# Kernel tuning notes

Measured on AMD Instinct MI355X. Metric: run time of the kernel, lower is better.

Reference implementation:

```python
import jax, jax.numpy as jnp
import numpy as np


def setup_inputs() -> dict:
    key = jax.random.key(0)
    k1, k2, k3, k4 = jax.random.split(key, 4)
    B, S, C = 16, 2048, 512
    x = jax.random.normal(k1, (B, S, C), dtype=jnp.float32)
    x_prime = jax.random.normal(k2, (B, S, C), dtype=jnp.float32)
    W = jax.random.normal(k3, (C, C), dtype=jnp.float32) * (1.0 / np.sqrt(C))
    b = jax.random.normal(k4, (C,), dtype=jnp.float32) * 0.01
    return {"x": x, "x_prime": x_prime, "W": W, "b": b}


def reference(x, x_prime, W, b):
    # q = Linear(x_prime): [B, S, C]
    q = jnp.einsum("bsc,dc->bsd", x_prime, W) + b
    # score = tanh(x_prime) @ q^T : [B, S, S]
    score = jnp.einsum("bsc,btc->bst", jnp.tanh(x_prime), q)
    alpha = jax.nn.softmax(score, axis=-1)
    # y_att = alpha @ x : [B, S, C]
    y_att = jnp.einsum("bst,btc->bsc", alpha, x)
    # dropout is identity in eval mode
    return jnp.tanh(y_att)
```

## Files before the change

kernel.cpp:

```cpp
#include <hip/hip_runtime.h>
#include <hip/hip_bf16.h>
#include <math.h>

typedef __bf16 bf16x8 __attribute__((ext_vector_type(8)));
typedef float  f32x4  __attribute__((ext_vector_type(4)));
typedef float  f32x16 __attribute__((ext_vector_type(16)));

#define MFMA16(a, b, c) __builtin_amdgcn_mfma_f32_16x16x32_bf16((a), (b), (c), 0, 0, 0)
#define MFMA32(a, b, c) __builtin_amdgcn_mfma_f32_32x32x16_bf16((a), (b), (c), 0, 0, 0)

static constexpr int    kB  = 16;
static constexpr int    kS  = 2048;
static constexpr int    kC  = 512;
static constexpr size_t kNE = (size_t)kB * kS * kC;

static __device__ __forceinline__ void split_bf16(float v, __bf16 &hi, __bf16 &lo) {
  hi = (__bf16)v;
  lo = (__bf16)(v - (float)hi);
}

static __device__ __forceinline__ int swzb(int row, int e) {
  return ((row << 7) + (e << 1)) ^ ((row & 7) << 4);
}
static __device__ __forceinline__ int swzp(int row, int e) {
  return ((row << 8) + (e << 1)) ^ ((row & 7) << 4);
}

static __device__ __forceinline__ void split_store16_swz(
    float4 v0, float4 v1, float4 v2, float4 v3, char* hi, char* lo, int row, int e0) {
  float vv[16] = {v0.x, v0.y, v0.z, v0.w, v1.x, v1.y, v1.z, v1.w,
                  v2.x, v2.y, v2.z, v2.w, v3.x, v3.y, v3.z, v3.w};
  bf16x8 h0, h1, l0, l1;
#pragma unroll
  for (int i = 0; i < 8; ++i) {
    __bf16 a, b;
    split_bf16(vv[i], a, b);     h0[i] = a; l0[i] = b;
    split_bf16(vv[8 + i], a, b); h1[i] = a; l1[i] = b;
  }
  *(bf16x8*)(hi + swzb(row, e0))     = h0;
  *(bf16x8*)(hi + swzb(row, e0 + 8)) = h1;
  *(bf16x8*)(lo + swzb(row, e0))     = l0;
  *(bf16x8*)(lo + swzb(row, e0 + 8)) = l1;
}

__global__ __launch_bounds__(256) void k_tanh_split(
    const float* __restrict__ xp, __bf16* __restrict__ th, __bf16* __restrict__ tl) {
  size_t i = ((size_t)blockIdx.x * 256 + threadIdx.x) * 8;
  float4 a = *(const float4*)(xp + i);
  float4 b = *(const float4*)(xp + i + 4);
  float v[8] = {a.x, a.y, a.z, a.w, b.x, b.y, b.z, b.w};
  bf16x8 h, l;
#pragma unroll
  for (int k = 0; k < 8; ++k) {
    float t = tanhf(v[k]);
    __bf16 hh, ll;
    split_bf16(t, hh, ll);
    h[k] = hh; l[k] = ll;
  }
  *(bf16x8*)(th + i) = h;
  *(bf16x8*)(tl + i) = l;
}

__global__ __launch_bounds__(256) void k_transpose_x(
    const float* __restrict__ x, __bf16* __restrict__ xbt) {
  __shared__ float tile[64][65];
  int bid = blockIdx.x;
  int b   = bid >> 8;
  int t0  = ((bid >> 3) & 31) * 64;
  int c0  = (bid & 7) * 64;
  int row = threadIdx.x >> 2;
  int seg = threadIdx.x & 3;
  const float* src = x + (size_t)(b * kS + t0 + row) * kC + c0 + seg * 16;
  float4 v0 = *(const float4*)(src + 0);
  float4 v1 = *(const float4*)(src + 4);
  float4 v2 = *(const float4*)(src + 8);
  float4 v3 = *(const float4*)(src + 12);
  float vv[16] = {v0.x, v0.y, v0.z, v0.w, v1.x, v1.y, v1.z, v1.w,
                  v2.x, v2.y, v2.z, v2.w, v3.x, v3.y, v3.z, v3.w};
#pragma unroll
  for (int i = 0; i < 16; ++i) tile[row][seg * 16 + i] = vv[i];
  __syncthreads();
  bf16x8 o0, o1;
#pragma unroll
  for (int i = 0; i < 8; ++i) o0[i] = (__bf16)tile[seg * 16 + i][row];
#pragma unroll
  for (int i = 0; i < 8; ++i) o1[i] = (__bf16)tile[seg * 16 + 8 + i][row];
  __bf16* dst = xbt + (size_t)(b * kC + c0 + row) * kS + t0 + seg * 16;
  *(bf16x8*)(dst)     = o0;
  *(bf16x8*)(dst + 8) = o1;
}

__global__ __launch_bounds__(256) void k_qgemm(
    const float* __restrict__ xp, const float* __restrict__ W,
    const float* __restrict__ bias, __bf16* __restrict__ qh, __bf16* __restrict__ ql) {
  __shared__ __align__(16) char lds[32768];
  char* Ah = lds;
  char* Al = lds + 8192;
  char* Bh = lds + 16384;
  char* Bl = lds + 24576;

  int bid = blockIdx.x;
  int n0  = (bid & 7) * 64;
  int m0  = (bid >> 3) * 64;

  int tid  = threadIdx.x;
  int lane = tid & 63;
  int wave = tid >> 6;
  int qd   = lane >> 4;
  int cl   = lane & 15;
  int row  = tid >> 2;
  int seg  = tid & 3;

  f32x4 acc[4] = {};
  const float* srcA = xp + (size_t)(m0 + row) * kC + seg * 16;
  const float* srcB = W  + (size_t)(n0 + row) * kC + seg * 16;

  float4 va0, va1, va2, va3, vb0, vb1, vb2, vb3;
  auto load_ab = [&](int kc) {
    const float* a = srcA + kc * 64;
    va0 = *(const float4*)(a);      va1 = *(const float4*)(a + 4);
    va2 = *(const float4*)(a + 8);  va3 = *(const float4*)(a + 12);
    const float* bb = srcB + kc * 64;
    vb0 = *(const float4*)(bb);     vb1 = *(const float4*)(bb + 4);
    vb2 = *(const float4*)(bb + 8); vb3 = *(const float4*)(bb + 12);
  };

  load_ab(0);
  for (int kc = 0; kc < 8; ++kc) {
    split_store16_swz(va0, va1, va2, va3, Ah, Al, row, seg * 16);
    split_store16_swz(vb0, vb1, vb2, vb3, Bh, Bl, row, seg * 16);
    __syncthreads();
    if (kc < 7) load_ab(kc + 1);
    __builtin_amdgcn_s_setprio(1);
#pragma unroll
    for (int ks = 0; ks < 2; ++ks) {
      int ka = ks * 32 + qd * 8;
      bf16x8 ah = *(const bf16x8*)(Ah + swzb(wave * 16 + cl, ka));
      bf16x8 al = *(const bf16x8*)(Al + swzb(wave * 16 + cl, ka));
#pragma unroll
      for (int j = 0; j < 4; ++j) {
        bf16x8 bh = *(const bf16x8*)(Bh + swzb(j * 16 + cl, ka));
        bf16x8 bl = *(const bf16x8*)(Bl + swzb(j * 16 + cl, ka));
        acc[j] = MFMA16(ah, bh, acc[j]);
        acc[j] = MFMA16(ah, bl, acc[j]);
        acc[j] = MFMA16(al, bh, acc[j]);
      }
    }
    __builtin_amdgcn_s_setprio(0);
    __syncthreads();
  }
#pragma unroll
  for (int j = 0; j < 4; ++j) {
    int d = n0 + j * 16 + cl;
    float bv = bias[d];
#pragma unroll
    for (int r = 0; r < 4; ++r) {
      int m = m0 + wave * 16 + qd * 4 + r;
      float v = acc[j][r] + bv;
      __bf16 h, l;
      split_bf16(v, h, l);
      qh[(size_t)m * kC + d] = h;
      ql[(size_t)m * kC + d] = l;
    }
  }
}

__global__ __launch_bounds__(256, 2) void k_attn(
    const __bf16* __restrict__ th, const __bf16* __restrict__ tl,
    const __bf16* __restrict__ qh, const __bf16* __restrict__ ql,
    const __bf16* __restrict__ xbt, float* __restrict__ out) {
  __shared__ __align__(16) char lds[49664];
  char* Ah  = lds;
  char* Al  = lds + 8192;
  char* Bh  = lds + 16384;
  char* Bl  = lds + 32768;
  char* P   = lds;
  char* Xt0 = lds + 16384;
  char* Xt1 = lds + 32768;
  float* stat = (float*)(lds + 49152);

  int bid = blockIdx.x;
  int b   = (bid & 7) | ((bid >> 8) << 3);
  int s0  = ((bid >> 3) & 31) * 64;

  int tid  = threadIdx.x;
  int lane = tid & 63;
  int wave = tid >> 6;
  int qd   = lane >> 4;
  int cl   = lane & 15;
  int l31  = lane & 31;
  int lh   = lane >> 5;
  int whalf = wave & 1;
  int wcol  = wave >> 1;

  const float LOG2E = 1.4426950408889634f;

  float m_r[4], l_r[4];
  f32x16 O[8] = {};
#pragma unroll
  for (int r = 0; r < 4; ++r) { m_r[r] = -INFINITY; l_r[r] = 0.f; }

  const size_t rowbase = (size_t)b * kS;

  const int arow = tid >> 2, aseg = tid & 3;
  const int brow = tid >> 1, bseg = tid & 1;
  const int xrow = tid >> 2, xseg = tid & 3;
  const int prow = whalf * 32 + l31;

  for (int tt = 0; tt < 16; ++tt) {
    int t0 = tt * 128;
    f32x4 Sacc[8] = {};
    for (int kc = 0; kc < 8; ++kc) {
      {
        size_t g = (rowbase + s0 + arow) * kC + kc * 64 + aseg * 16;
        bf16x8 h0 = *(const bf16x8*)(th + g), h1 = *(const bf16x8*)(th + g + 8);
        bf16x8 l0 = *(const bf16x8*)(tl + g), l1 = *(const bf16x8*)(tl + g + 8);
        *(bf16x8*)(Ah + swzb(arow, aseg * 16))     = h0;
        *(bf16x8*)(Ah + swzb(arow, aseg * 16 + 8)) = h1;
        *(bf16x8*)(Al + swzb(arow, aseg * 16))     = l0;
        *(bf16x8*)(Al + swzb(arow, aseg * 16 + 8)) = l1;
      }
      {
        size_t g = (rowbase + t0 + brow) * kC + kc * 64 + bseg * 32;
#pragma unroll
        for (int u = 0; u < 4; ++u) {
          bf16x8 vh = *(const bf16x8*)(qh + g + u * 8);
          bf16x8 vl = *(const bf16x8*)(ql + g + u * 8);
          *(bf16x8*)(Bh + swzb(brow, bseg * 32 + u * 8)) = vh;
          *(bf16x8*)(Bl + swzb(brow, bseg * 32 + u * 8)) = vl;
        }
      }
      __syncthreads();
      __builtin_amdgcn_s_setprio(1);
#pragma unroll
      for (int ks = 0; ks < 2; ++ks) {
        int ka = ks * 32 + qd * 8;
        bf16x8 ah = *(const bf16x8*)(Ah + swzb(wave * 16 + cl, ka));
        bf16x8 al = *(const bf16x8*)(Al + swzb(wave * 16 + cl, ka));
#pragma unroll
        for (int j = 0; j < 8; ++j) {
          bf16x8 bh = *(const bf16x8*)(Bh + swzb(j * 16 + cl, ka));
          bf16x8 bl = *(const bf16x8*)(Bl + swzb(j * 16 + cl, ka));
          Sacc[j] = MFMA16(ah, bh, Sacc[j]);
          Sacc[j] = MFMA16(ah, bl, Sacc[j]);
          Sacc[j] = MFMA16(al, bh, Sacc[j]);
        }
      }
      __builtin_amdgcn_s_setprio(0);
      __syncthreads();
    }
    float rmax[4];
#pragma unroll
    for (int r = 0; r < 4; ++r) {
      float v = Sacc[0][r];
#pragma unroll
      for (int j = 1; j < 8; ++j) v = fmaxf(v, Sacc[j][r]);
      rmax[r] = v;
    }
#pragma unroll
    for (int mk = 1; mk < 16; mk <<= 1)
#pragma unroll
      for (int r = 0; r < 4; ++r)
        rmax[r] = fmaxf(rmax[r], __shfl_xor(rmax[r], mk, 64));
    float alpha[4], rsum[4];
#pragma unroll
    for (int r = 0; r < 4; ++r) {
      float mn = fmaxf(m_r[r], rmax[r]);
      alpha[r] = exp2f((m_r[r] - mn) * LOG2E);
      m_r[r] = mn;
      rsum[r] = 0.f;
    }
#pragma unroll
    for (int j = 0; j < 8; ++j)
#pragma unroll
      for (int r = 0; r < 4; ++r) {
        float p = exp2f((Sacc[j][r] - m_r[r]) * LOG2E);
        Sacc[j][r] = p;
        rsum[r] += p;
      }
#pragma unroll
    for (int mk = 1; mk < 16; mk <<= 1)
#pragma unroll
      for (int r = 0; r < 4; ++r)
        rsum[r] += __shfl_xor(rsum[r], mk, 64);
#pragma unroll
    for (int r = 0; r < 4; ++r)
      l_r[r] = l_r[r] * alpha[r] + rsum[r];
    if (cl == 0) {
#pragma unroll
      for (int r = 0; r < 4; ++r) stat[wave * 16 + qd * 4 + r] = alpha[r];
    }
#pragma unroll
    for (int j = 0; j < 8; ++j)
#pragma unroll
      for (int r = 0; r < 4; ++r) {
        int pr = wave * 16 + qd * 4 + r;
        *(__bf16*)(P + swzp(pr, j * 16 + cl)) = (__bf16)Sacc[j][r];
      }
    __syncthreads();
    float ar[16];
#pragma unroll
    for (int i = 0; i < 16; ++i)
      ar[i] = stat[whalf * 32 + (i & 3) + 8 * (i >> 2) + 4 * lh];
    bf16x8 pa[8];
#pragma unroll
    for (int ks = 0; ks < 8; ++ks)
      pa[ks] = *(const bf16x8*)(P + swzp(prow, ks * 16 + lh * 8));
#pragma unroll
    for (int t = 0; t < 8; ++t)
#pragma unroll
      for (int i = 0; i < 16; ++i)
        O[t][i] *= ar[i];
#pragma unroll
    for (int step = 0; step < 4; ++step) {
      {
        size_t g0 = ((size_t)b * kC + step * 64 + xrow) * kS + t0 + xseg * 32;
        size_t g1 = g0 + (size_t)256 * kS;
#pragma unroll
        for (int u = 0; u < 4; ++u)
          *(bf16x8*)(Xt0 + swzp(xrow, xseg * 32 + u * 8)) = *(const bf16x8*)(xbt + g0 + u * 8);
#pragma unroll
        for (int u = 0; u < 4; ++u)
          *(bf16x8*)(Xt1 + swzp(xrow, xseg * 32 + u * 8)) = *(const bf16x8*)(xbt + g1 + u * 8);
      }
      __syncthreads();
      const char* Xt = wcol ? Xt1 : Xt0;
      __builtin_amdgcn_s_setprio(1);
#pragma unroll
      for (int ks = 0; ks < 8; ++ks) {
#pragma unroll
        for (int nloc = 0; nloc < 2; ++nloc) {
          bf16x8 xb = *(const bf16x8*)(Xt + swzp(nloc * 32 + l31, ks * 16 + lh * 8));
          O[step * 2 + nloc] = MFMA32(pa[ks], xb, O[step * 2 + nloc]);
        }
      }
      __builtin_amdgcn_s_setprio(0);
      __syncthreads();
    }
  }
  if (cl == 0) {
#pragma unroll
    for (int r = 0; r < 4; ++r) stat[wave * 16 + qd * 4 + r] = l_r[r];
  }
  __syncthreads();
  float linv[16];
#pragma unroll
  for (int i = 0; i < 16; ++i)
    linv[i] = __builtin_amdgcn_rcpf(stat[whalf * 32 + (i & 3) + 8 * (i >> 2) + 4 * lh]);
#pragma unroll
  for (int t = 0; t < 8; ++t) {
    int colbase = wcol * 256 + (t >> 1) * 64 + (t & 1) * 32 + l31;
#pragma unroll
    for (int i = 0; i < 16; ++i) {
      int rowl = (i & 3) + 8 * (i >> 2) + 4 * lh;
      float v = O[t][i] * linv[i];
      float e = exp2f(2.f * LOG2E * v);
      out[(rowbase + s0 + whalf * 32 + rowl) * kC + colbase] =
          1.f - 2.f * __builtin_amdgcn_rcpf(e + 1.f);
    }
  }
}

extern "C" void kernel_launch(void* const* d_in, const int* in_sizes, int n_in,
                              void* d_out, int out_size, void* d_ws, size_t ws_size,
                              hipStream_t stream) {
  const float* x    = (const float*)d_in[0];
  const float* xp   = (const float*)d_in[1];
  const float* W    = (const float*)d_in[2];
  const float* bias = (const float*)d_in[3];
  float* out = (float*)d_out;

  __bf16* ws  = (__bf16*)d_ws;
  __bf16* th  = ws;
  __bf16* tl  = ws + kNE;
  __bf16* qh  = ws + 2 * kNE;
  __bf16* ql  = ws + 3 * kNE;
  __bf16* xbt = ws + 4 * kNE;

  k_tanh_split<<<8192, 256, 0, stream>>>(xp, th, tl);
  k_transpose_x<<<4096, 256, 0, stream>>>(x, xbt);
  k_qgemm<<<4096, 256, 0, stream>>>(xp, W, bias, qh, ql);
  k_attn<<<512, 256, 0, stream>>>(th, tl, qh, ql, xbt, out);
}
```

Baseline: 1.090 ms.

## Restructure attention kernel with async global-to-LDS double buffering and larger tiles

Rewrites the fused attention kernel to use 512-thread blocks covering 128 query rows, with direct global-to-LDS loads (global_load_lds) that are double-buffered so the next K-chunk and X tiles are fetched while the current MFMAs run. The score GEMM moves from 16x16 to 32x32 MFMA tiles, and row max/sum are combined across wave pairs through LDS. The goal is to hide memory latency and cut register-staged copies and synchronization stalls. In exchange it uses about 160KB of LDS, which limits occupancy, and it launches only 256 blocks, which risks underfilling the GPU.

```diff
diff --git a/kernel.cpp b/kernel.cpp
--- a/kernel.cpp
+++ b/kernel.cpp
@@ -19,11 +19,14 @@
   lo = (__bf16)(v - (float)hi);
 }
 
+static __device__ __forceinline__ void gload16(const void* g, void* l) {
+  __builtin_amdgcn_global_load_lds(
+      (const __attribute__((address_space(1))) char*)g,
+      (__attribute__((address_space(3))) char*)l, 16, 0, 0);
+}
+
 static __device__ __forceinline__ int swzb(int row, int e) {
   return ((row << 7) + (e << 1)) ^ ((row & 7) << 4);
-}
-static __device__ __forceinline__ int swzp(int row, int e) {
-  return ((row << 8) + (e << 1)) ^ ((row & 7) << 4);
 }
 
 static __device__ __forceinline__ void split_store16_swz(
@@ -165,197 +168,203 @@
   }
 }
 
-__global__ __launch_bounds__(256, 2) void k_attn(
+__global__ __launch_bounds__(512, 2) void k_attn(
     const __bf16* __restrict__ th, const __bf16* __restrict__ tl,
     const __bf16* __restrict__ qh, const __bf16* __restrict__ ql,
     const __bf16* __restrict__ xbt, float* __restrict__ out) {
-  __shared__ __align__(16) char lds[49664];
-  char* Ah  = lds;
-  char* Al  = lds + 8192;
-  char* Bh  = lds + 16384;
-  char* Bl  = lds + 32768;
-  char* P   = lds;
-  char* Xt0 = lds + 16384;
-  char* Xt1 = lds + 32768;
-  float* stat = (float*)(lds + 49152);
+  __shared__ __align__(16) char lds[163840];
+  char*  P     = lds + 65536;
+  float* statm = (float*)(lds);
+  float* stats = (float*)(lds + 1024);
+  const int XEVEN = 98304, XODD = 131072;
 
   int bid = blockIdx.x;
-  int b   = (bid & 7) | ((bid >> 8) << 3);
-  int s0  = ((bid >> 3) & 31) * 64;
+  int b   = bid >> 4;
+  int s0  = (bid & 15) * 128;
 
   int tid  = threadIdx.x;
   int lane = tid & 63;
-  int wave = tid >> 6;
-  int qd   = lane >> 4;
-  int cl   = lane & 15;
+  int wv   = tid >> 6;
   int l31  = lane & 31;
   int lh   = lane >> 5;
-  int whalf = wave & 1;
-  int wcol  = wave >> 1;
+  int wg   = wv >> 1;
+  int cg   = wv & 1;
 
   const float LOG2E = 1.4426950408889634f;
 
-  float m_r[4], l_r[4];
+  float m_r[16], l_r[16];
+#pragma unroll
+  for (int i = 0; i < 16; ++i) { m_r[i] = -INFINITY; l_r[i] = 0.f; }
   f32x16 O[8] = {};
-#pragma unroll
-  for (int r = 0; r < 4; ++r) { m_r[r] = -INFINITY; l_r[r] = 0.f; }
-
-  const size_t rowbase = (size_t)b * kS;
-
-  const int arow = tid >> 2, aseg = tid & 3;
-  const int brow = tid >> 1, bseg = tid & 1;
-  const int xrow = tid >> 2, xseg = tid & 3;
-  const int prow = whalf * 32 + l31;
+
+  auto stage_score = [&](int kc, int bufsel, int t0q) {
+    char* Ahd = lds + bufsel * 65536;
+    char* Ald = Ahd + 16384;
+    char* Bhd = Ahd + 32768;
+    char* Bld = Ahd + 49152;
+#pragma unroll
+    for (int u = 0; u < 2; ++u) {
+      int slot = wv * 128 + u * 64 + lane;
+      int r = slot >> 3;
+      int c = (slot & 7) ^ (r & 7);
+      size_t gA = (size_t)(b * kS + s0 + r) * kC + kc * 64 + c * 8;
+      size_t gB = (size_t)(b * kS + t0q + r) * kC + kc * 64 + c * 8;
+      int ldoff = (wv * 128 + u * 64) * 16;
+      gload16(th + gA, Ahd + ldoff);
+      gload16(tl + gA, Ald + ldoff);
+      gload16(qh + gB, Bhd + ldoff);
+      gload16(ql + gB, Bld + ldoff);
+    }
+  };
+  auto stage_xpair = [&](int step, int pairbase, int t0q) {
+#pragma unroll
+    for (int half = 0; half < 2; ++half) {
+      char* dst = lds + pairbase + half * 16384;
+#pragma unroll
+      for (int u = 0; u < 2; ++u) {
+        int slot = wv * 128 + u * 64 + lane;
+        int r = slot >> 4;
+        int c = (slot & 15) ^ (r & 7);
+        size_t g = ((size_t)b * kC + half * 256 + step * 64 + r) * kS + t0q + c * 8;
+        gload16(xbt + g, dst + (wv * 128 + u * 64) * 16);
+      }
+    }
+  };
+
+  stage_score(0, 0, 0);
+  __syncthreads();
+
+  const int arow = wg * 32 + l31;
+  const int prow = wg * 32 + l31;
 
   for (int tt = 0; tt < 16; ++tt) {
     int t0 = tt * 128;
-    f32x4 Sacc[8] = {};
+    f32x16 S0 = {}, S1 = {};
     for (int kc = 0; kc < 8; ++kc) {
-      {
-        size_t g = (rowbase + s0 + arow) * kC + kc * 64 + aseg * 16;
-        bf16x8 h0 = *(const bf16x8*)(th + g), h1 = *(const bf16x8*)(th + g + 8);
-        bf16x8 l0 = *(const bf16x8*)(tl + g), l1 = *(const bf16x8*)(tl + g + 8);
-        *(bf16x8*)(Ah + swzb(arow, aseg * 16))     = h0;
-        *(bf16x8*)(Ah + swzb(arow, aseg * 16 + 8)) = h1;
-        *(bf16x8*)(Al + swzb(arow, aseg * 16))     = l0;
-        *(bf16x8*)(Al + swzb(arow, aseg * 16 + 8)) = l1;
-      }
-      {
-        size_t g = (rowbase + t0 + brow) * kC + kc * 64 + bseg * 32;
-#pragma unroll
-        for (int u = 0; u < 4; ++u) {
-          bf16x8 vh = *(const bf16x8*)(qh + g + u * 8);
-          bf16x8 vl = *(const bf16x8*)(ql + g + u * 8);
-          *(bf16x8*)(Bh + swzb(brow, bseg * 32 + u * 8)) = vh;
-          *(bf16x8*)(Bl + swzb(brow, bseg * 32 + u * 8)) = vl;
-        }
-      }
-      __syncthreads();
+      if (kc < 7) stage_score(kc + 1, (kc + 1) & 1, t0);
+      const char* cb  = lds + (kc & 1) * 65536;
+      const char* cAh = cb, *cAl = cb + 16384, *cBh = cb + 32768, *cBl = cb + 49152;
       __builtin_amdgcn_s_setprio(1);
 #pragma unroll
-      for (int ks = 0; ks < 2; ++ks) {
-        int ka = ks * 32 + qd * 8;
-        bf16x8 ah = *(const bf16x8*)(Ah + swzb(wave * 16 + cl, ka));
-        bf16x8 al = *(const bf16x8*)(Al + swzb(wave * 16 + cl, ka));
-#pragma unroll
-        for (int j = 0; j < 8; ++j) {
-          bf16x8 bh = *(const bf16x8*)(Bh + swzb(j * 16 + cl, ka));
-          bf16x8 bl = *(const bf16x8*)(Bl + swzb(j * 16 + cl, ka));
-          Sacc[j] = MFMA16(ah, bh, Sacc[j]);
-          Sacc[j] = MFMA16(ah, bl, Sacc[j]);
-          Sacc[j] = MFMA16(al, bh, Sacc[j]);
+      for (int ks = 0; ks < 4; ++ks) {
+        int ach = ((ks * 2 + lh) ^ (arow & 7)) * 16;
+        bf16x8 ah = *(const bf16x8*)(cAh + arow * 128 + ach);
+        bf16x8 al = *(const bf16x8*)(cAl + arow * 128 + ach);
+#pragma unroll
+        for (int tile = 0; tile < 2; ++tile) {
+          int trow = cg * 64 + tile * 32 + l31;
+          int bch  = ((ks * 2 + lh) ^ (trow & 7)) * 16;
+          bf16x8 bh = *(const bf16x8*)(cBh + trow * 128 + bch);
+          bf16x8 bl = *(const bf16x8*)(cBl + trow * 128 + bch);
+          if (tile == 0) {
+            S0 = MFMA32(ah, bh, S0); S0 = MFMA32(ah, bl, S0); S0 = MFMA32(al, bh, S0);
+          } else {
+            S1 = MFMA32(ah, bh, S1); S1 = MFMA32(ah, bl, S1); S1 = MFMA32(al, bh, S1);
+          }
         }
       }
       __builtin_amdgcn_s_setprio(0);
       __syncthreads();
     }
-    float rmax[4];
-#pragma unroll
-    for (int r = 0; r < 4; ++r) {
-      float v = Sacc[0][r];
-#pragma unroll
-      for (int j = 1; j < 8; ++j) v = fmaxf(v, Sacc[j][r]);
-      rmax[r] = v;
-    }
-#pragma unroll
-    for (int mk = 1; mk < 16; mk <<= 1)
-#pragma unroll
-      for (int r = 0; r < 4; ++r)
-        rmax[r] = fmaxf(rmax[r], __shfl_xor(rmax[r], mk, 64));
-    float alpha[4], rsum[4];
-#pragma unroll
-    for (int r = 0; r < 4; ++r) {
-      float mn = fmaxf(m_r[r], rmax[r]);
-      alpha[r] = exp2f((m_r[r] - mn) * LOG2E);
-      m_r[r] = mn;
-      rsum[r] = 0.f;
+    float rm[16];
+#pragma unroll
+    for (int i = 0; i < 16; ++i) rm[i] = fmaxf(S0[i], S1[i]);
+#pragma unroll
+    for (int mk = 1; mk < 32; mk <<= 1)
+#pragma unroll
+      for (int i = 0; i < 16; ++i) rm[i] = fmaxf(rm[i], __shfl_xor(rm[i], mk, 64));
+    if (l31 == 0) {
+#pragma unroll
+      for (int i = 0; i < 16; ++i) {
+        int rl = (i & 3) + 8 * (i >> 2) + 4 * lh;
+        statm[cg * 128 + wg * 32 + rl] = rm[i];
+      }
+    }
+    __syncthreads();
+    stage_xpair(0, XEVEN, t0);
+    float alpha[16];
+#pragma unroll
+    for (int i = 0; i < 16; ++i) {
+      int rl = (i & 3) + 8 * (i >> 2) + 4 * lh;
+      float om = statm[(cg ^ 1) * 128 + wg * 32 + rl];
+      float M  = fmaxf(m_r[i], fmaxf(rm[i], om));
+      alpha[i] = exp2f((m_r[i] - M) * LOG2E);
+      m_r[i] = M;
+      l_r[i] *= alpha[i];
     }
 #pragma unroll
     for (int j = 0; j < 8; ++j)
 #pragma unroll
-      for (int r = 0; r < 4; ++r) {
-        float p = exp2f((Sacc[j][r] - m_r[r]) * LOG2E);
-        Sacc[j][r] = p;
-        rsum[r] += p;
-      }
-#pragma unroll
-    for (int mk = 1; mk < 16; mk <<= 1)
-#pragma unroll
-      for (int r = 0; r < 4; ++r)
-        rsum[r] += __shfl_xor(rsum[r], mk, 64);
-#pragma unroll
-    for (int r = 0; r < 4; ++r)
-      l_r[r] = l_r[r] * alpha[r] + rsum[r];
-    if (cl == 0) {
-#pragma unroll
-      for (int r = 0; r < 4; ++r) stat[wave * 16 + qd * 4 + r] = alpha[r];
-    }
-#pragma unroll
-    for (int j = 0; j < 8; ++j)
-#pragma unroll
-      for (int r = 0; r < 4; ++r) {
-        int pr = wave * 16 + qd * 4 + r;
-        *(__bf16*)(P + swzp(pr, j * 16 + cl)) = (__bf16)Sacc[j][r];
-      }
-    __syncthreads();
-    float ar[16];
-#pragma unroll
-    for (int i = 0; i < 16; ++i)
-      ar[i] = stat[whalf * 32 + (i & 3) + 8 * (i >> 2) + 4 * lh];
+      for (int i = 0; i < 16; ++i) O[j][i] *= alpha[i];
+    float rs[16];
+#pragma unroll
+    for (int i = 0; i < 16; ++i) {
+      S0[i] = exp2f((S0[i] - m_r[i]) * LOG2E);
+      S1[i] = exp2f((S1[i] - m_r[i]) * LOG2E);
+      rs[i] = S0[i] + S1[i];
+    }
+#pragma unroll
+    for (int mk = 1; mk < 32; mk <<= 1)
+#pragma unroll
+      for (int i = 0; i < 16; ++i) rs[i] += __shfl_xor(rs[i], mk, 64);
+    if (l31 == 0) {
+#pragma unroll
+      for (int i = 0; i < 16; ++i) {
+        int rl = (i & 3) + 8 * (i >> 2) + 4 * lh;
+        stats[cg * 128 + wg * 32 + rl] = rs[i];
+      }
+    }
+#pragma unroll
+    for (int tile = 0; tile < 2; ++tile)
+#pragma unroll
+      for (int i = 0; i < 16; ++i) {
+        int s = wg * 32 + (i & 3) + 8 * (i >> 2) + 4 * lh;
+        int t = cg * 64 + tile * 32 + l31;
+        int off = s * 256 + ((((t >> 3) ^ (s & 7)) << 4) | ((t & 7) << 1));
+        *(__bf16*)(P + off) = (__bf16)(tile ? S1[i] : S0[i]);
+      }
+    __syncthreads();
+#pragma unroll
+    for (int i = 0; i < 16; ++i) {
+      int rl = (i & 3) + 8 * (i >> 2) + 4 * lh;
+      l_r[i] += rs[i] + stats[(cg ^ 1) * 128 + wg * 32 + rl];
+    }
     bf16x8 pa[8];
 #pragma unroll
-    for (int ks = 0; ks < 8; ++ks)
-      pa[ks] = *(const bf16x8*)(P + swzp(prow, ks * 16 + lh * 8));
-#pragma unroll
-    for (int t = 0; t < 8; ++t)
-#pragma unroll
-      for (int i = 0; i < 16; ++i)
-        O[t][i] *= ar[i];
+    for (int ks = 0; ks < 8; ++ks) {
+      int ch = ((ks * 2 + lh) ^ (prow & 7)) * 16;
+      pa[ks] = *(const bf16x8*)(P + prow * 256 + ch);
+    }
+    __syncthreads();
 #pragma unroll
     for (int step = 0; step < 4; ++step) {
-      {
-        size_t g0 = ((size_t)b * kC + step * 64 + xrow) * kS + t0 + xseg * 32;
-        size_t g1 = g0 + (size_t)256 * kS;
-#pragma unroll
-        for (int u = 0; u < 4; ++u)
-          *(bf16x8*)(Xt0 + swzp(xrow, xseg * 32 + u * 8)) = *(const bf16x8*)(xbt + g0 + u * 8);
-#pragma unroll
-        for (int u = 0; u < 4; ++u)
-          *(bf16x8*)(Xt1 + swzp(xrow, xseg * 32 + u * 8)) = *(const bf16x8*)(xbt + g1 + u * 8);
-      }
-      __syncthreads();
-      const char* Xt = wcol ? Xt1 : Xt0;
+      if (step < 3)      stage_xpair(step + 1, ((step + 1) & 1) ? XODD : XEVEN, t0);
+      else if (tt < 15)  stage_score(0, 0, t0 + 128);
+      const char* xbb = lds + ((step & 1) ? XODD : XEVEN) + cg * 16384;
       __builtin_amdgcn_s_setprio(1);
 #pragma unroll
-      for (int ks = 0; ks < 8; ++ks) {
-#pragma unroll
-        for (int nloc = 0; nloc < 2; ++nloc) {
-          bf16x8 xb = *(const bf16x8*)(Xt + swzp(nloc * 32 + l31, ks * 16 + lh * 8));
-          O[step * 2 + nloc] = MFMA32(pa[ks], xb, O[step * 2 + nloc]);
+      for (int ks = 0; ks < 8; ++ks)
+#pragma unroll
+        for (int tile = 0; tile < 2; ++tile) {
+          int xrow = tile * 32 + l31;
+          int ch = ((ks * 2 + lh) ^ (xrow & 7)) * 16;
+          bf16x8 xb = *(const bf16x8*)(xbb + xrow * 256 + ch);
+          O[step * 2 + tile] = MFMA32(pa[ks], xb, O[step * 2 + tile]);
         }
-      }
       __builtin_amdgcn_s_setprio(0);
       __syncthreads();
     }
   }
-  if (cl == 0) {
-#pragma unroll
-    for (int r = 0; r < 4; ++r) stat[wave * 16 + qd * 4 + r] = l_r[r];
-  }
-  __syncthreads();
-  float linv[16];
-#pragma unroll
-  for (int i = 0; i < 16; ++i)
-    linv[i] = __builtin_amdgcn_rcpf(stat[whalf * 32 + (i & 3) + 8 * (i >> 2) + 4 * lh]);
-#pragma unroll
-  for (int t = 0; t < 8; ++t) {
-    int colbase = wcol * 256 + (t >> 1) * 64 + (t & 1) * 32 + l31;
-#pragma unroll
-    for (int i = 0; i < 16; ++i) {
-      int rowl = (i & 3) + 8 * (i >> 2) + 4 * lh;
-      float v = O[t][i] * linv[i];
+#pragma unroll
+  for (int i = 0; i < 16; ++i) {
+    int rl = (i & 3) + 8 * (i >> 2) + 4 * lh;
+    float inv = __builtin_amdgcn_rcpf(l_r[i]);
+    size_t rowoff = ((size_t)b * kS + s0 + wg * 32 + rl) * kC;
+#pragma unroll
+    for (int j = 0; j < 8; ++j) {
+      float v = O[j][i] * inv;
       float e = exp2f(2.f * LOG2E * v);
-      out[(rowbase + s0 + whalf * 32 + rowl) * kC + colbase] =
+      out[rowoff + cg * 256 + (j >> 1) * 64 + (j & 1) * 32 + l31] =
           1.f - 2.f * __builtin_amdgcn_rcpf(e + 1.f);
     }
   }
@@ -380,5 +389,5 @@
   k_tanh_split<<<8192, 256, 0, stream>>>(xp, th, tl);
   k_transpose_x<<<4096, 256, 0, stream>>>(x, xbt);
   k_qgemm<<<4096, 256, 0, stream>>>(xp, W, bias, qh, ql);
-  k_attn<<<512, 256, 0, stream>>>(th, tl, qh, ql, xbt, out);
-}
+  k_attn<<<256, 512, 0, stream>>>(th, tl, qh, ql, xbt, out);
+}
```

Result: slower. 1.124 ms (+3.1%).

## Switch attention to fp16 MFMA with two-term Q split and retiled waves

Applied to the files above, without the earlier changes.

Moves all intermediate operands from bf16 to fp16. tanh(x') is now stored as a single fp16 value, and Q keeps a hi/lo split, so the score GEMM needs two MFMAs per tile instead of three, and the tanh low-part buffer is dropped. The attention kernel is retiled so each wave computes a 64x32 score slice and a 64x128 output slice with 16x16x32 f16 MFMAs. Row max and row sum are now combined across waves through LDS, which adds an extra barrier. Accuracy now depends on fp16 range and the reduced split precision.

```diff
diff --git a/kernel.cpp b/kernel.cpp
--- a/kernel.cpp
+++ b/kernel.cpp
@@ -2,12 +2,12 @@
 #include <hip/hip_bf16.h>
 #include <math.h>
 
-typedef __bf16 bf16x8 __attribute__((ext_vector_type(8)));
-typedef float  f32x4  __attribute__((ext_vector_type(4)));
-typedef float  f32x16 __attribute__((ext_vector_type(16)));
+typedef __bf16    bf16x8 __attribute__((ext_vector_type(8)));
+typedef _Float16  f16x8  __attribute__((ext_vector_type(8)));
+typedef float     f32x4  __attribute__((ext_vector_type(4)));
 
 #define MFMA16(a, b, c) __builtin_amdgcn_mfma_f32_16x16x32_bf16((a), (b), (c), 0, 0, 0)
-#define MFMA32(a, b, c) __builtin_amdgcn_mfma_f32_32x32x16_bf16((a), (b), (c), 0, 0, 0)
+#define MFMAH(a, b, c)  __builtin_amdgcn_mfma_f32_16x16x32_f16((a), (b), (c), 0, 0, 0)
 
 static constexpr int    kB  = 16;
 static constexpr int    kS  = 2048;
@@ -21,9 +21,6 @@
 
 static __device__ __forceinline__ int swzb(int row, int e) {
   return ((row << 7) + (e << 1)) ^ ((row & 7) << 4);
-}
-static __device__ __forceinline__ int swzp(int row, int e) {
-  return ((row << 8) + (e << 1)) ^ ((row & 7) << 4);
 }
 
 static __device__ __forceinline__ void split_store16_swz(
@@ -43,26 +40,20 @@
   *(bf16x8*)(lo + swzb(row, e0 + 8)) = l1;
 }
 
-__global__ __launch_bounds__(256) void k_tanh_split(
-    const float* __restrict__ xp, __bf16* __restrict__ th, __bf16* __restrict__ tl) {
+__global__ __launch_bounds__(256) void k_tanh_f16(
+    const float* __restrict__ xp, _Float16* __restrict__ th) {
   size_t i = ((size_t)blockIdx.x * 256 + threadIdx.x) * 8;
   float4 a = *(const float4*)(xp + i);
   float4 b = *(const float4*)(xp + i + 4);
   float v[8] = {a.x, a.y, a.z, a.w, b.x, b.y, b.z, b.w};
-  bf16x8 h, l;
-#pragma unroll
-  for (int k = 0; k < 8; ++k) {
-    float t = tanhf(v[k]);
-    __bf16 hh, ll;
-    split_bf16(t, hh, ll);
-    h[k] = hh; l[k] = ll;
-  }
-  *(bf16x8*)(th + i) = h;
-  *(bf16x8*)(tl + i) = l;
+  f16x8 h;
+#pragma unroll
+  for (int k = 0; k < 8; ++k) h[k] = (_Float16)tanhf(v[k]);
+  *(f16x8*)(th + i) = h;
 }
 
 __global__ __launch_bounds__(256) void k_transpose_x(
-    const float* __restrict__ x, __bf16* __restrict__ xbt) {
+    const float* __restrict__ x, _Float16* __restrict__ xbt) {
   __shared__ float tile[64][65];
   int bid = blockIdx.x;
   int b   = bid >> 8;
@@ -80,19 +71,19 @@
 #pragma unroll
   for (int i = 0; i < 16; ++i) tile[row][seg * 16 + i] = vv[i];
   __syncthreads();
-  bf16x8 o0, o1;
-#pragma unroll
-  for (int i = 0; i < 8; ++i) o0[i] = (__bf16)tile[seg * 16 + i][row];
-#pragma unroll
-  for (int i = 0; i < 8; ++i) o1[i] = (__bf16)tile[seg * 16 + 8 + i][row];
-  __bf16* dst = xbt + (size_t)(b * kC + c0 + row) * kS + t0 + seg * 16;
-  *(bf16x8*)(dst)     = o0;
-  *(bf16x8*)(dst + 8) = o1;
+  f16x8 o0, o1;
+#pragma unroll
+  for (int i = 0; i < 8; ++i) o0[i] = (_Float16)tile[seg * 16 + i][row];
+#pragma unroll
+  for (int i = 0; i < 8; ++i) o1[i] = (_Float16)tile[seg * 16 + 8 + i][row];
+  _Float16* dst = xbt + (size_t)(b * kC + c0 + row) * kS + t0 + seg * 16;
+  *(f16x8*)(dst)     = o0;
+  *(f16x8*)(dst + 8) = o1;
 }
 
 __global__ __launch_bounds__(256) void k_qgemm(
     const float* __restrict__ xp, const float* __restrict__ W,
-    const float* __restrict__ bias, __bf16* __restrict__ qh, __bf16* __restrict__ ql) {
+    const float* __restrict__ bias, _Float16* __restrict__ qh, _Float16* __restrict__ ql) {
   __shared__ __align__(16) char lds[32768];
   char* Ah = lds;
   char* Al = lds + 8192;
@@ -157,8 +148,8 @@
     for (int r = 0; r < 4; ++r) {
       int m = m0 + wave * 16 + qd * 4 + r;
       float v = acc[j][r] + bv;
-      __bf16 h, l;
-      split_bf16(v, h, l);
+      _Float16 h = (_Float16)v;
+      _Float16 l = (_Float16)(v - (float)h);
       qh[(size_t)m * kC + d] = h;
       ql[(size_t)m * kC + d] = l;
     }
@@ -166,199 +157,219 @@
 }
 
 __global__ __launch_bounds__(256, 2) void k_attn(
-    const __bf16* __restrict__ th, const __bf16* __restrict__ tl,
-    const __bf16* __restrict__ qh, const __bf16* __restrict__ ql,
-    const __bf16* __restrict__ xbt, float* __restrict__ out) {
-  __shared__ __align__(16) char lds[49664];
-  char* Ah  = lds;
-  char* Al  = lds + 8192;
-  char* Bh  = lds + 16384;
-  char* Bl  = lds + 32768;
-  char* P   = lds;
-  char* Xt0 = lds + 16384;
-  char* Xt1 = lds + 32768;
-  float* stat = (float*)(lds + 49152);
+    const _Float16* __restrict__ th, const _Float16* __restrict__ qh,
+    const _Float16* __restrict__ ql, const _Float16* __restrict__ xbt,
+    float* __restrict__ out) {
+  __shared__ __align__(16) char lds[59392];
+  char*  Ta    = lds;
+  char*  Qh    = lds + 8192;
+  char*  Ql    = lds + 24576;
+  char*  Xt    = lds;
+  char*  P     = lds + 40960;
+  float* statm = (float*)(lds + 57344);
+  float* stats = (float*)(lds + 58368);
 
   int bid = blockIdx.x;
-  int b   = (bid & 7) | ((bid >> 8) << 3);
-  int s0  = ((bid >> 3) & 31) * 64;
+  int swz = (bid & 7) * 64 + (bid >> 3);
+  int b   = swz >> 5;
+  int s0  = (swz & 31) * 64;
 
   int tid  = threadIdx.x;
   int lane = tid & 63;
-  int wave = tid >> 6;
+  int wv   = tid >> 6;
   int qd   = lane >> 4;
   int cl   = lane & 15;
-  int l31  = lane & 31;
-  int lh   = lane >> 5;
-  int whalf = wave & 1;
-  int wcol  = wave >> 1;
 
   const float LOG2E = 1.4426950408889634f;
 
-  float m_r[4], l_r[4];
-  f32x16 O[8] = {};
-#pragma unroll
-  for (int r = 0; r < 4; ++r) { m_r[r] = -INFINITY; l_r[r] = 0.f; }
-
-  const size_t rowbase = (size_t)b * kS;
-
-  const int arow = tid >> 2, aseg = tid & 3;
-  const int brow = tid >> 1, bseg = tid & 1;
-  const int xrow = tid >> 2, xseg = tid & 3;
-  const int prow = whalf * 32 + l31;
+  float m_r[16], l_r[16];
+#pragma unroll
+  for (int i = 0; i < 16; ++i) { m_r[i] = -INFINITY; l_r[i] = 0.f; }
+  f32x4 O[4][8] = {};
+
+  auto stage_score = [&](int kc, int t0) {
+    {
+      int ar = tid >> 2, as = tid & 3;
+      const _Float16* ga = th + (size_t)(b * kS + s0 + ar) * kC + kc * 64 + as * 16;
+      f16x8 a0 = *(const f16x8*)ga;
+      f16x8 a1 = *(const f16x8*)(ga + 8);
+      *(f16x8*)(Ta + ar * 128 + (((as * 2)     ^ (ar & 7)) << 4)) = a0;
+      *(f16x8*)(Ta + ar * 128 + (((as * 2 + 1) ^ (ar & 7)) << 4)) = a1;
+    }
+    {
+      int qr = tid >> 1, qs = tid & 1;
+      size_t gq = (size_t)(b * kS + t0 + qr) * kC + kc * 64 + qs * 32;
+#pragma unroll
+      for (int u = 0; u < 4; ++u) {
+        f16x8 vh = *(const f16x8*)(qh + gq + u * 8);
+        f16x8 vl = *(const f16x8*)(ql + gq + u * 8);
+        int cc = (((qs * 4 + u) ^ (qr & 7)) << 4);
+        *(f16x8*)(Qh + qr * 128 + cc) = vh;
+        *(f16x8*)(Ql + qr * 128 + cc) = vl;
+      }
+    }
+  };
+  auto stage_x = [&](int sub, int t0) {
+#pragma unroll
+    for (int u = 0; u < 2; ++u) {
+      int r = tid * 2 + u;
+      const _Float16* gx = xbt + (size_t)(b * kC + r) * kS + t0 + sub * 32;
+#pragma unroll
+      for (int j = 0; j < 4; ++j) {
+        f16x8 v = *(const f16x8*)(gx + j * 8);
+        int cc = ((j ^ (r & 3) ^ ((r >> 2) & 3)) << 4);
+        *(f16x8*)(Xt + r * 64 + cc) = v;
+      }
+    }
+  };
 
   for (int tt = 0; tt < 16; ++tt) {
     int t0 = tt * 128;
-    f32x4 Sacc[8] = {};
+    f32x4 S[4][2] = {};
     for (int kc = 0; kc < 8; ++kc) {
-      {
-        size_t g = (rowbase + s0 + arow) * kC + kc * 64 + aseg * 16;
-        bf16x8 h0 = *(const bf16x8*)(th + g), h1 = *(const bf16x8*)(th + g + 8);
-        bf16x8 l0 = *(const bf16x8*)(tl + g), l1 = *(const bf16x8*)(tl + g + 8);
-        *(bf16x8*)(Ah + swzb(arow, aseg * 16))     = h0;
-        *(bf16x8*)(Ah + swzb(arow, aseg * 16 + 8)) = h1;
-        *(bf16x8*)(Al + swzb(arow, aseg * 16))     = l0;
-        *(bf16x8*)(Al + swzb(arow, aseg * 16 + 8)) = l1;
-      }
-      {
-        size_t g = (rowbase + t0 + brow) * kC + kc * 64 + bseg * 32;
-#pragma unroll
-        for (int u = 0; u < 4; ++u) {
-          bf16x8 vh = *(const bf16x8*)(qh + g + u * 8);
-          bf16x8 vl = *(const bf16x8*)(ql + g + u * 8);
-          *(bf16x8*)(Bh + swzb(brow, bseg * 32 + u * 8)) = vh;
-          *(bf16x8*)(Bl + swzb(brow, bseg * 32 + u * 8)) = vl;
-        }
-      }
+      stage_score(kc, t0);
       __syncthreads();
       __builtin_amdgcn_s_setprio(1);
 #pragma unroll
       for (int ks = 0; ks < 2; ++ks) {
-        int ka = ks * 32 + qd * 8;
-        bf16x8 ah = *(const bf16x8*)(Ah + swzb(wave * 16 + cl, ka));
-        bf16x8 al = *(const bf16x8*)(Al + swzb(wave * 16 + cl, ka));
-#pragma unroll
-        for (int j = 0; j < 8; ++j) {
-          bf16x8 bh = *(const bf16x8*)(Bh + swzb(j * 16 + cl, ka));
-          bf16x8 bl = *(const bf16x8*)(Bl + swzb(j * 16 + cl, ka));
-          Sacc[j] = MFMA16(ah, bh, Sacc[j]);
-          Sacc[j] = MFMA16(ah, bl, Sacc[j]);
-          Sacc[j] = MFMA16(al, bh, Sacc[j]);
+        f16x8 ta[4], qbh[2], qbl[2];
+#pragma unroll
+        for (int mt = 0; mt < 4; ++mt) {
+          int rr = mt * 16 + cl;
+          ta[mt] = *(const f16x8*)(Ta + rr * 128 + ((((ks * 4 + qd) ^ (rr & 7))) << 4));
         }
+#pragma unroll
+        for (int nt = 0; nt < 2; ++nt) {
+          int rr = wv * 32 + nt * 16 + cl;
+          int cc = ((((ks * 4 + qd) ^ (rr & 7))) << 4);
+          qbh[nt] = *(const f16x8*)(Qh + rr * 128 + cc);
+          qbl[nt] = *(const f16x8*)(Ql + rr * 128 + cc);
+        }
+#pragma unroll
+        for (int mt = 0; mt < 4; ++mt)
+#pragma unroll
+          for (int nt = 0; nt < 2; ++nt) {
+            S[mt][nt] = MFMAH(ta[mt], qbh[nt], S[mt][nt]);
+            S[mt][nt] = MFMAH(ta[mt], qbl[nt], S[mt][nt]);
+          }
       }
       __builtin_amdgcn_s_setprio(0);
       __syncthreads();
     }
-    float rmax[4];
-#pragma unroll
-    for (int r = 0; r < 4; ++r) {
-      float v = Sacc[0][r];
-#pragma unroll
-      for (int j = 1; j < 8; ++j) v = fmaxf(v, Sacc[j][r]);
-      rmax[r] = v;
-    }
+    float rm[16];
+#pragma unroll
+    for (int mt = 0; mt < 4; ++mt)
+#pragma unroll
+      for (int r = 0; r < 4; ++r)
+        rm[mt * 4 + r] = fmaxf(S[mt][0][r], S[mt][1][r]);
 #pragma unroll
     for (int mk = 1; mk < 16; mk <<= 1)
 #pragma unroll
-      for (int r = 0; r < 4; ++r)
-        rmax[r] = fmaxf(rmax[r], __shfl_xor(rmax[r], mk, 64));
-    float alpha[4], rsum[4];
-#pragma unroll
-    for (int r = 0; r < 4; ++r) {
-      float mn = fmaxf(m_r[r], rmax[r]);
-      alpha[r] = exp2f((m_r[r] - mn) * LOG2E);
-      m_r[r] = mn;
-      rsum[r] = 0.f;
-    }
-#pragma unroll
-    for (int j = 0; j < 8; ++j)
+      for (int i = 0; i < 16; ++i) rm[i] = fmaxf(rm[i], __shfl_xor(rm[i], mk, 64));
+    if (cl == 0) {
+#pragma unroll
+      for (int mt = 0; mt < 4; ++mt)
+#pragma unroll
+        for (int r = 0; r < 4; ++r)
+          statm[(mt * 16 + qd * 4 + r) * 4 + wv] = rm[mt * 4 + r];
+    }
+    __syncthreads();
+    float alpha[16];
+#pragma unroll
+    for (int mt = 0; mt < 4; ++mt)
 #pragma unroll
       for (int r = 0; r < 4; ++r) {
-        float p = exp2f((Sacc[j][r] - m_r[r]) * LOG2E);
-        Sacc[j][r] = p;
-        rsum[r] += p;
+        int i = mt * 4 + r;
+        f32x4 pm = *(const f32x4*)&statm[(mt * 16 + qd * 4 + r) * 4];
+        float M = fmaxf(fmaxf(fmaxf(pm[0], pm[1]), fmaxf(pm[2], pm[3])), m_r[i]);
+        alpha[i] = exp2f((m_r[i] - M) * LOG2E);
+        m_r[i] = M;
+      }
+    float rs[16];
+#pragma unroll
+    for (int mt = 0; mt < 4; ++mt)
+#pragma unroll
+      for (int r = 0; r < 4; ++r) {
+        int i = mt * 4 + r;
+        float p0 = exp2f((S[mt][0][r] - m_r[i]) * LOG2E);
+        float p1 = exp2f((S[mt][1][r] - m_r[i]) * LOG2E);
+        S[mt][0][r] = p0; S[mt][1][r] = p1;
+        rs[i] = p0 + p1;
       }
 #pragma unroll
     for (int mk = 1; mk < 16; mk <<= 1)
 #pragma unroll
-      for (int r = 0; r < 4; ++r)
-        rsum[r] += __shfl_xor(rsum[r], mk, 64);
-#pragma unroll
-    for (int r = 0; r < 4; ++r)
-      l_r[r] = l_r[r] * alpha[r] + rsum[r];
+      for (int i = 0; i < 16; ++i) rs[i] += __shfl_xor(rs[i], mk, 64);
     if (cl == 0) {
 #pragma unroll
-      for (int r = 0; r < 4; ++r) stat[wave * 16 + qd * 4 + r] = alpha[r];
-    }
-#pragma unroll
-    for (int j = 0; j < 8; ++j)
+      for (int mt = 0; mt < 4; ++mt)
+#pragma unroll
+        for (int r = 0; r < 4; ++r)
+          stats[(mt * 16 + qd * 4 + r) * 4 + wv] = rs[mt * 4 + r];
+    }
+#pragma unroll
+    for (int mt = 0; mt < 4; ++mt)
+#pragma unroll
+      for (int nt = 0; nt < 2; ++nt)
+#pragma unroll
+        for (int r = 0; r < 4; ++r) {
+          int row = mt * 16 + qd * 4 + r;
+          int col = wv * 32 + nt * 16 + cl;
+          int off = row * 256 + ((((col >> 3) ^ (row & 7)) << 4)) + ((col & 7) << 1);
+          *(_Float16*)(P + off) = (_Float16)S[mt][nt][r];
+        }
+#pragma unroll
+    for (int mt = 0; mt < 4; ++mt)
+#pragma unroll
+      for (int nt = 0; nt < 8; ++nt)
+#pragma unroll
+        for (int r = 0; r < 4; ++r)
+          O[mt][nt][r] *= alpha[mt * 4 + r];
+    __syncthreads();
+#pragma unroll
+    for (int mt = 0; mt < 4; ++mt)
 #pragma unroll
       for (int r = 0; r < 4; ++r) {
-        int pr = wave * 16 + qd * 4 + r;
-        *(__bf16*)(P + swzp(pr, j * 16 + cl)) = (__bf16)Sacc[j][r];
-      }
-    __syncthreads();
-    float ar[16];
-#pragma unroll
-    for (int i = 0; i < 16; ++i)
-      ar[i] = stat[whalf * 32 + (i & 3) + 8 * (i >> 2) + 4 * lh];
-    bf16x8 pa[8];
-#pragma unroll
-    for (int ks = 0; ks < 8; ++ks)
-      pa[ks] = *(const bf16x8*)(P + swzp(prow, ks * 16 + lh * 8));
-#pragma unroll
-    for (int t = 0; t < 8; ++t)
-#pragma unroll
-      for (int i = 0; i < 16; ++i)
-        O[t][i] *= ar[i];
-#pragma unroll
-    for (int step = 0; step < 4; ++step) {
-      {
-        size_t g0 = ((size_t)b * kC + step * 64 + xrow) * kS + t0 + xseg * 32;
-        size_t g1 = g0 + (size_t)256 * kS;
-#pragma unroll
-        for (int u = 0; u < 4; ++u)
-          *(bf16x8*)(Xt0 + swzp(xrow, xseg * 32 + u * 8)) = *(const bf16x8*)(xbt + g0 + u * 8);
-#pragma unroll
-        for (int u = 0; u < 4; ++u)
-          *(bf16x8*)(Xt1 + swzp(xrow, xseg * 32 + u * 8)) = *(const bf16x8*)(xbt + g1 + u * 8);
-      }
+        int i = mt * 4 + r;
+        f32x4 ps = *(const f32x4*)&stats[(mt * 16 + qd * 4 + r) * 4];
+        l_r[i] = l_r[i] * alpha[i] + (ps[0] + ps[1] + ps[2] + ps[3]);
+      }
+#pragma unroll
+    for (int sub = 0; sub < 4; ++sub) {
+      stage_x(sub, t0);
       __syncthreads();
-      const char* Xt = wcol ? Xt1 : Xt0;
+      f16x8 pa[4];
+#pragma unroll
+      for (int mt = 0; mt < 4; ++mt) {
+        int row = mt * 16 + cl;
+        pa[mt] = *(const f16x8*)(P + row * 256 + ((((sub * 4 + qd) ^ (row & 7))) << 4));
+      }
       __builtin_amdgcn_s_setprio(1);
 #pragma unroll
-      for (int ks = 0; ks < 8; ++ks) {
-#pragma unroll
-        for (int nloc = 0; nloc < 2; ++nloc) {
-          bf16x8 xb = *(const bf16x8*)(Xt + swzp(nloc * 32 + l31, ks * 16 + lh * 8));
-          O[step * 2 + nloc] = MFMA32(pa[ks], xb, O[step * 2 + nloc]);
-        }
+      for (int nt = 0; nt < 8; ++nt) {
+        int xr = wv * 128 + nt * 16 + cl;
+        f16x8 xb = *(const f16x8*)(Xt + xr * 64 + ((qd ^ (xr & 3) ^ ((xr >> 2) & 3)) << 4));
+#pragma unroll
+        for (int mt = 0; mt < 4; ++mt)
+          O[mt][nt] = MFMAH(pa[mt], xb, O[mt][nt]);
       }
       __builtin_amdgcn_s_setprio(0);
       __syncthreads();
     }
   }
-  if (cl == 0) {
-#pragma unroll
-    for (int r = 0; r < 4; ++r) stat[wave * 16 + qd * 4 + r] = l_r[r];
-  }
-  __syncthreads();
-  float linv[16];
-#pragma unroll
-  for (int i = 0; i < 16; ++i)
-    linv[i] = __builtin_amdgcn_rcpf(stat[whalf * 32 + (i & 3) + 8 * (i >> 2) + 4 * lh]);
-#pragma unroll
-  for (int t = 0; t < 8; ++t) {
-    int colbase = wcol * 256 + (t >> 1) * 64 + (t & 1) * 32 + l31;
-#pragma unroll
-    for (int i = 0; i < 16; ++i) {
-      int rowl = (i & 3) + 8 * (i >> 2) + 4 * lh;
-      float v = O[t][i] * linv[i];
-      float e = exp2f(2.f * LOG2E * v);
-      out[(rowbase + s0 + whalf * 32 + rowl) * kC + colbase] =
-          1.f - 2.f * __builtin_amdgcn_rcpf(e + 1.f);
-    }
-  }
+#pragma unroll
+  for (int mt = 0; mt < 4; ++mt)
+#pragma unroll
+    for (int r = 0; r < 4; ++r) {
+      float inv = __builtin_amdgcn_rcpf(l_r[mt * 4 + r]);
+      size_t ro = (size_t)(b * kS + s0 + mt * 16 + qd * 4 + r) * kC + wv * 128;
+#pragma unroll
+      for (int nt = 0; nt < 8; ++nt) {
+        float v = O[mt][nt][r] * inv;
+        float e = exp2f(2.f * LOG2E * v);
+        out[ro + nt * 16 + cl] = 1.f - 2.f * __builtin_amdgcn_rcpf(e + 1.f);
+      }
+    }
 }
 
 extern "C" void kernel_launch(void* const* d_in, const int* in_sizes, int n_in,
@@ -370,15 +381,14 @@
   const float* bias = (const float*)d_in[3];
   float* out = (float*)d_out;
 
-  __bf16* ws  = (__bf16*)d_ws;
-  __bf16* th  = ws;
-  __bf16* tl  = ws + kNE;
-  __bf16* qh  = ws + 2 * kNE;
-  __bf16* ql  = ws + 3 * kNE;
-  __bf16* xbt = ws + 4 * kNE;
-
-  k_tanh_split<<<8192, 256, 0, stream>>>(xp, th, tl);
+  _Float16* ws  = (_Float16*)d_ws;
+  _Float16* th  = ws;
+  _Float16* qh  = ws + kNE;
+  _Float16* ql  = ws + 2 * kNE;
+  _Float16* xbt = ws + 3 * kNE;
+
+  k_tanh_f16<<<8192, 256, 0, stream>>>(xp, th);
   k_transpose_x<<<4096, 256, 0, stream>>>(x, xbt);
   k_qgemm<<<4096, 256, 0, stream>>>(xp, W, bias, qh, ql);
-  k_attn<<<512, 256, 0, stream>>>(th, tl, qh, ql, xbt, out);
-}
+  k_attn<<<512, 256, 0, stream>>>(th, qh, ql, xbt, out);
+}
```

Measured after the change: 1.233 ms. 1.13x slower.
